# Optimization experiments

Hardware: AMD Instinct MI355X
Metric: run time of the kernel (lower is better)

Reference implementation:

```python
import jax, jax.numpy as jnp
import numpy as np

B = 8192
EPS = 1e-5  # BatchNorm eps (torch default)


def binarize(x):
    # sign binarization with straight-through estimator (matches the .data trick
    # in BinarizeConv2d/BinarizeLinear: forward sees +-1, backward sees identity)
    s = jnp.where(x >= 0, 1.0, -1.0).astype(x.dtype)
    return x + jax.lax.stop_gradient(s - x)


def conv2d(x, w, stride, pad):
    return jax.lax.conv_general_dilated(
        x, w, window_strides=stride, padding=pad,
        dimension_numbers=('NCHW', 'OIHW', 'NCHW'))


def bn(x, g, b, m, v):
    # eval-mode BatchNorm2d folded into one scale+shift per channel
    inv = g * jax.lax.rsqrt(v + EPS)
    return x * inv[None, :, None, None] + (b - m * inv)[None, :, None, None]


def maxpool_w2(x):
    # MaxPool2d(kernel=(1,2), stride=(1,2))
    return jax.lax.reduce_window(x, -jnp.inf, jax.lax.max,
                                 (1, 1, 1, 2), (1, 1, 1, 2), 'VALID')


def setup_inputs() -> dict:
    key = jax.random.key(0)
    ks = jax.random.split(key, 32)
    d = {}
    d['x'] = jax.random.normal(ks[0], (B, 1, 6, 128), jnp.float32)

    def w(k, shape):
        return jax.random.normal(k, shape, jnp.float32) * 0.05

    # conv weights (OIHW) and biases
    d['w1'] = w(ks[1], (32, 1, 1, 9));    d['b1'] = w(ks[2], (32,))
    d['w2'] = w(ks[3], (64, 32, 1, 3));   d['b2'] = w(ks[4], (64,))
    d['w3'] = w(ks[5], (128, 64, 1, 3));  d['b3'] = w(ks[6], (128,))
    d['w4'] = w(ks[7], (128, 128, 6, 1)); d['b4'] = w(ks[8], (128,))
    # BatchNorm params (gamma, beta, running_mean, running_var)
    for i, c in zip((1, 2, 3, 4), (32, 64, 128, 128)):
        kk = jax.random.split(ks[8 + i], 4)
        d[f'g{i}'] = 1.0 + 0.1 * jax.random.normal(kk[0], (c,), jnp.float32)
        d[f'be{i}'] = 0.1 * jax.random.normal(kk[1], (c,), jnp.float32)
        d[f'm{i}'] = 0.1 * jax.random.normal(kk[2], (c,), jnp.float32)
        d[f'v{i}'] = jax.random.uniform(kk[3], (c,), jnp.float32, 0.5, 1.5)
    # fc: BinarizeLinear(2048, 10)
    d['wf'] = w(ks[20], (10, 2048))
    d['bf'] = w(ks[21], (10,))
    return d


def reference(x, w1, b1, w2, b2, w3, b3, w4, b4,
              g1, be1, m1, v1, g2, be2, m2, v2,
              g3, be3, m3, v3, g4, be4, m4, v4, wf, bf):
    # block 1: first layer keeps real-valued input, binarized weights
    h = conv2d(x, binarize(w1), (1, 2), [(0, 0), (4, 4)]) + b1[None, :, None, None]
    h = jnp.clip(bn(h, g1, be1, m1, v1), -1.0, 1.0)   # Hardtanh
    h = maxpool_w2(h)                                  # [B,32,6,32]
    # block 2: binarized activations + weights
    h = conv2d(binarize(h), binarize(w2), (1, 1), [(0, 0), (1, 1)]) + b2[None, :, None, None]
    h = jnp.clip(bn(h, g2, be2, m2, v2), -1.0, 1.0)    # [B,64,6,32]
    # block 3
    h = conv2d(binarize(h), binarize(w3), (1, 1), [(0, 0), (1, 1)]) + b3[None, :, None, None]
    h = jnp.clip(bn(h, g3, be3, m3, v3), -1.0, 1.0)
    h = maxpool_w2(h)                                  # [B,128,6,16]
    # block 4: (6,1) kernel collapses H
    h = conv2d(binarize(h), binarize(w4), (1, 1), [(0, 0), (0, 0)]) + b4[None, :, None, None]
    h = jnp.clip(bn(h, g4, be4, m4, v4), -1.0, 1.0)    # [B,128,1,16]
    h = h.reshape(h.shape[0], -1)                      # [B,2048]
    return binarize(h) @ binarize(wf).T + bf           # [B,10]
```

## Files before the change

kernel.cpp:

```cpp
#include <hip/hip_runtime.h>
#include <cstdint>
#include <cstddef>

#define BN_EPS 1e-5f
#define BATCH 8192

typedef unsigned long long u64;
typedef uint32_t u32;
typedef int v4i __attribute__((ext_vector_type(4)));
typedef int v16i __attribute__((ext_vector_type(16)));

__device__ __forceinline__ u32 f2k(float f) {
    u32 u = __float_as_uint(f);
    return (u >> 31) ? ~u : (u | 0x80000000u);
}
__device__ __forceinline__ float k2f(u32 k) {
    u32 u = (k & 0x80000000u) ? (k ^ 0x80000000u) : ~k;
    return __uint_as_float(u);
}
__device__ __forceinline__ float bn_eval(float conv, float B, float iv, float sh) {
    return __fadd_rn(__fmul_rn(__fadd_rn(conv, B), iv), sh);
}

__global__ __launch_bounds__(256) void prep_all(
    const float* w1, const float* b1, const float* w2, const float* b2,
    const float* w3, const float* b3, const float* w4, const float* b4,
    const float* wf,
    const float* g1, const float* be1, const float* m1, const float* v1,
    const float* g2, const float* be2, const float* m2, const float* v2,
    const float* g3, const float* be3, const float* m3, const float* v3,
    const float* g4, const float* be4, const float* m4, const float* v4,
    float* s1f, float* T1, u32* wt2w, int* T2,
    uint4* b3i8, int* C3, u64* wt4, int* T4, u64* wtf) {
    int t = blockIdx.x * 256 + threadIdx.x;

    if (t < 384) {
        int co = t / 12, k = t % 12;
        float val = 0.f;
        if (k < 9) {
            float iv = g1[co] * rsqrtf(v1[co] + BN_EPS);
            float d = (iv < 0.f) ? -1.f : 1.f;
            val = ((w1[co * 9 + k] >= 0.f) ? 1.f : -1.f) * d;
        }
        s1f[t] = val;
    } else if (t < 416) {
        int co = t - 384;
        float iv = g1[co] * rsqrtf(v1[co] + BN_EPS);
        float sh = be1[co] - m1[co] * iv;
        float B = b1[co];
        bool flip = (iv < 0.f);
        auto pred = [&](float sp) {
            float sum = flip ? -sp : sp;
            return bn_eval(sum, B, iv, sh) >= 0.f;
        };
        u32 lo = f2k(-3.0e38f), hi = f2k(3.0e38f);
        float Tv;
        if (pred(k2f(lo))) Tv = k2f(lo);
        else if (!pred(k2f(hi))) Tv = __uint_as_float(0x7F800000u);
        else {
            while (hi - lo > 1u) {
                u32 mid = lo + ((hi - lo) >> 1);
                if (pred(k2f(mid))) hi = mid; else lo = mid;
            }
            Tv = k2f(hi);
        }
        T1[co] = Tv;
    } else if (t < 608) {
        int idx = t - 416;
        int co = idx / 3, kw = idx % 3;
        float iv = g2[co] * rsqrtf(v2[co] + BN_EPS);
        bool flip = (iv < 0.f);
        u32 wb = 0;
        for (int ci = 0; ci < 32; ++ci)
            wb |= (u32)((w2[(co * 32 + ci) * 3 + kw] >= 0.f) != flip) << ci;
        wt2w[co * 4 + kw] = wb;
    } else if (t < 800) {
        int idx = t - 608;
        int co = idx & 63, cls = idx >> 6;
        float iv = g2[co] * rsqrtf(v2[co] + BN_EPS);
        float sh = be2[co] - m2[co] * iv;
        float B = b2[co];
        bool flip = (iv < 0.f);
        int spur = 0, nv = 3;
        if (cls == 1) { nv = 2; for (int ci = 0; ci < 32; ++ci) spur += (int)((w2[(co * 32 + ci) * 3 + 0] >= 0.f) != flip); }
        if (cls == 2) { nv = 2; for (int ci = 0; ci < 32; ++ci) spur += (int)((w2[(co * 32 + ci) * 3 + 2] >= 0.f) != flip); }
        int maxp = 32 * nv + spur;
        int T = -1;
        for (int p = 0; p <= maxp; ++p) {
            int conv = flip ? (2 * (p - spur) - 32 * nv) : (32 * nv - 2 * (p - spur));
            float y = bn_eval((float)conv, B, iv, sh);
            if ((y >= 0.f) && (T == p - 1)) T = p;
        }
        T2[cls * 64 + co] = T;
    } else if (t < 2336) {
        int idx = t - 800;
        int q = idx >> 7, n = idx & 127;
        float iv = g3[n] * rsqrtf(v3[n] + BN_EPS);
        bool flip = (iv < 0.f);
        int kw = q >> 2, ci0 = (q & 3) * 16;
        u32 wd[4] = {0, 0, 0, 0};
        for (int j = 0; j < 16; ++j) {
            int ci = ci0 + j;
            bool pos = (w3[(n * 64 + ci) * 3 + kw] >= 0.f) != flip;
            u32 byte = pos ? 0x01u : 0xFFu;
            wd[j >> 2] |= byte << (8 * (j & 3));
        }
        b3i8[idx] = make_uint4(wd[0], wd[1], wd[2], wd[3]);
    } else if (t < 2464) {
        int co = t - 2336;
        float iv = g3[co] * rsqrtf(v3[co] + BN_EPS);
        float sh = be3[co] - m3[co] * iv;
        float B = b3[co];
        int C = 1000;
        if (iv >= 0.f) {
            for (int v = -192; v <= 192; v += 2)
                if (bn_eval((float)v, B, iv, sh) >= 0.f) { C = v; break; }
        } else {
            for (int v = 192; v >= -192; v -= 2)
                if (bn_eval((float)v, B, iv, sh) >= 0.f) { C = -v; break; }
        }
        C3[co] = C;
    } else if (t < 4000) {
        int idx = t - 2464;
        int j = idx & 1, ch = idx >> 1;
        int co = ch / 6, h = ch % 6;
        float iv = g4[co] * rsqrtf(v4[co] + BN_EPS);
        bool flip = (iv < 0.f);
        u64 wb = 0;
        for (int cb = 0; cb < 64; ++cb) {
            int ci = j * 64 + cb;
            wb |= (u64)((w4[(co * 128 + ci) * 6 + h] >= 0.f) != flip) << cb;
        }
        wt4[idx] = wb;
    } else if (t < 4128) {
        int co = t - 4000;
        float iv = g4[co] * rsqrtf(v4[co] + BN_EPS);
        float sh = be4[co] - m4[co] * iv;
        float B = b4[co];
        bool flip = (iv < 0.f);
        int T = -1;
        for (int p = 0; p <= 768; ++p) {
            int conv = flip ? (2 * p - 768) : (768 - 2 * p);
            float y = bn_eval((float)conv, B, iv, sh);
            if ((y >= 0.f) && (T == p - 1)) T = p;
        }
        T4[co] = T;
    } else if (t < 4448) {
        int idx = t - 4128;
        int o = idx / 32, wi = idx % 32;
        u64 wb = 0;
        for (int fb = 0; fb < 64; ++fb)
            wb |= (u64)(wf[o * 2048 + wi * 64 + fb] >= 0.f) << fb;
        wtf[idx] = wb;
    }
}

#define L12_ROWS 8
__global__ __launch_bounds__(256) void layer12_kernel(
    const float* __restrict__ x, const float4* __restrict__ s1p, const float* __restrict__ T1,
    const uint4* __restrict__ wt2v, const int* __restrict__ T2, u64* __restrict__ a2) {
    __shared__ float4 sS[96];
    __shared__ float sT[32];
    __shared__ uint4 sW[64];
    __shared__ int sT2[192];
    __shared__ u32 sA1[L12_ROWS][32];
    int t = threadIdx.x;
    if (t < 96) sS[t] = s1p[t];
    if (t < 32) sT[t] = T1[t];
    if (t < 64) sW[t] = wt2v[t];
    if (t < 192) sT2[t] = T2[t];
    __syncthreads();

    int r = t >> 5, wp = t & 31;
    int bh = blockIdx.x * L12_ROWS + r;
    const float* xp = x + (size_t)bh * 128;
    float xv[11];
    int p0 = 4 * wp - 4;
#pragma unroll
    for (int j = 0; j < 11; ++j) {
        int p = p0 + j;
        xv[j] = (p >= 0 && p < 128) ? xp[p] : 0.f;
    }
    u32 word = 0;
#pragma unroll
    for (int co = 0; co < 32; ++co) {
        float4 wa = sS[co * 3 + 0];
        float4 wb = sS[co * 3 + 1];
        float wc = sS[co * 3 + 2].x;
        float sum0 = 0.f, sum1 = 0.f;
        sum0 = fmaf(wa.x, xv[0], sum0);  sum1 = fmaf(wa.x, xv[2], sum1);
        sum0 = fmaf(wa.y, xv[1], sum0);  sum1 = fmaf(wa.y, xv[3], sum1);
        sum0 = fmaf(wa.z, xv[2], sum0);  sum1 = fmaf(wa.z, xv[4], sum1);
        sum0 = fmaf(wa.w, xv[3], sum0);  sum1 = fmaf(wa.w, xv[5], sum1);
        sum0 = fmaf(wb.x, xv[4], sum0);  sum1 = fmaf(wb.x, xv[6], sum1);
        sum0 = fmaf(wb.y, xv[5], sum0);  sum1 = fmaf(wb.y, xv[7], sum1);
        sum0 = fmaf(wb.z, xv[6], sum0);  sum1 = fmaf(wb.z, xv[8], sum1);
        sum0 = fmaf(wb.w, xv[7], sum0);  sum1 = fmaf(wb.w, xv[9], sum1);
        sum0 = fmaf(wc,   xv[8], sum0);  sum1 = fmaf(wc,   xv[10], sum1);
        float Tt = sT[co];
        word |= (u32)((sum0 >= Tt) || (sum1 >= Tt)) << co;
    }
    sA1[r][wp] = word;
    __syncthreads();

    u32 am = sA1[r][wp];
    u32 al = (wp > 0) ? sA1[r][wp - 1] : 0u;
    u32 ar = (wp < 31) ? sA1[r][wp + 1] : 0u;
    const int* Tp = &sT2[(wp == 0) ? 64 : ((wp == 31) ? 128 : 0)];
    u64 word2 = 0;
#pragma unroll
    for (int co = 0; co < 64; ++co) {
        uint4 wv = sW[co];
        int p = __popc(al ^ wv.x) + __popc(am ^ wv.y) + __popc(ar ^ wv.z);
        word2 |= (u64)(p <= Tp[co]) << co;
    }
    a2[(size_t)bh * 32 + wp] = word2;
}

#define L3_ROWS 4
__global__ __launch_bounds__(256) void layer3_mfma(
    const u64* __restrict__ a2, const uint4* __restrict__ b3i8, const int* __restrict__ C3,
    u32* __restrict__ a3u32) {
    __shared__ uint4 sB[12 * 128];
    __shared__ u64 sLUT[256];
    __shared__ int sC3[128];
    int t = threadIdx.x;
    for (int i = t; i < 1536; i += 256) sB[i] = b3i8[i];
    {
        u32 b = t & 255;
        u64 e = 0;
#pragma unroll
        for (int j = 0; j < 8; ++j)
            e |= (((b >> j) & 1) ? 0x01ull : 0xFFull) << (8 * j);
        if (t < 256) sLUT[t] = e;
    }
    if (t < 128) sC3[t] = C3[t];
    __syncthreads();

    int wv = t >> 6, lane = t & 63, m = lane & 31, half = lane >> 5;
    int rowBase = (blockIdx.x * 4 + wv) * L3_ROWS;
    const int prTab[8] = {0, 1, 4, 5, 8, 9, 12, 13};

    for (int r = 0; r < L3_ROWS; ++r) {
        int bh = rowBase + r;
        u64 aw = a2[(size_t)bh * 32 + m];
        u64 wm1 = __shfl(aw, m - 1);
        u64 wp1 = __shfl(aw, m + 1);

        v4i A[6];
#pragma unroll
        for (int kk = 0; kk < 6; ++kk) {
            const int kw = kk >> 1;
            u64 word = (kw == 0) ? wm1 : ((kw == 1) ? aw : wp1);
            bool valid = !((kw == 0 && m == 0) || (kw == 2 && m == 31));
            int ci0 = ((kk & 1) << 5) + (half << 4);
            u32 bits = (u32)(word >> ci0) & 0xFFFFu;
            u64 lo = sLUT[bits & 0xFF];
            u64 hi = sLUT[bits >> 8];
            if (!valid) { lo = 0; hi = 0; }
            union { u64 q[2]; v4i v; } u;
            u.q[0] = lo; u.q[1] = hi;
            A[kk] = u.v;
        }

        u32 outv = 0;
#pragma unroll
        for (int nt = 0; nt < 4; ++nt) {
            v16i acc;
#pragma unroll
            for (int i = 0; i < 16; ++i) acc[i] = 0;
#pragma unroll
            for (int kk = 0; kk < 6; ++kk) {
                int q = kk * 2 + half;
                union { uint4 u4; v4i v; } bu;
                bu.u4 = sB[q * 128 + nt * 32 + m];
                acc = __builtin_amdgcn_mfma_i32_32x32x32_i8(A[kk], bu.v, acc, 0, 0, 0);
            }
            int tc = sC3[nt * 32 + m];
#pragma unroll
            for (int rp = 0; rp < 8; ++rp) {
                bool c = (acc[2 * rp] >= tc) || (acc[2 * rp + 1] >= tc);
                u64 mk = __ballot(c);
                int LA = (nt << 4) | prTab[rp];
                int LB = LA + 2;
                outv = (lane == LA) ? (u32)mk : outv;
                outv = (lane == LB) ? (u32)(mk >> 32) : outv;
            }
        }
        a3u32[(size_t)bh * 64 + ((lane & 15) << 2) + (lane >> 4)] = outv;
    }
}

__global__ __launch_bounds__(256) void layer4_fc_kernel(
    const u64* __restrict__ a3, const u64* __restrict__ wt4, const int* __restrict__ T4,
    const u64* __restrict__ wtf, const float* __restrict__ bf, float* __restrict__ out) {
    __shared__ u64 sW4[1536];
    __shared__ u64 sWf[320];
    __shared__ u64 sFeat[16][32];
    __shared__ int sT[128];
    __shared__ float sBf[10];
    int t = threadIdx.x;
    {
        ulonglong2* d = (ulonglong2*)sW4;
        const ulonglong2* s = (const ulonglong2*)wt4;
        for (int i = t; i < 768; i += 256) d[i] = s[i];
        ulonglong2* df = (ulonglong2*)sWf;
        const ulonglong2* sf = (const ulonglong2*)wtf;
        if (t < 160) df[t] = sf[t];
    }
    if (t < 128) sT[t] = T4[t];
    if (t < 10) sBf[t] = bf[t];
    __syncthreads();
    int bb = t >> 4, w = t & 15, lane = t & 63, g = lane >> 4;
    int b = blockIdx.x * 16 + bb;
    u64 av[12];
#pragma unroll
    for (int h = 0; h < 6; ++h) {
        av[h * 2 + 0] = a3[(size_t)b * 192 + h * 32 + w * 2 + 0];
        av[h * 2 + 1] = a3[(size_t)b * 192 + h * 32 + w * 2 + 1];
    }
    u64 acc = 0;
#pragma unroll 8
    for (int co = 0; co < 128; ++co) {
        const u64* wr = &sW4[co * 12];
        int p = 0;
#pragma unroll
        for (int q = 0; q < 12; ++q) p += __popcll(av[q] ^ wr[q]);
        u64 m = __ballot(p <= sT[co]);
        u64 field = (m >> (g * 16)) & 0xFFFFull;
        acc |= field << ((co & 3) << 4);
        if ((co & 3) == 3) {
            if (w == 0) sFeat[bb][co >> 2] = acc;
            acc = 0;
        }
    }
    __syncthreads();
    if (t < 160) {
        int fb = t / 10, o = t % 10;
        int p = 0;
#pragma unroll
        for (int wi = 0; wi < 32; ++wi) p += __popcll(sFeat[fb][wi] ^ sWf[o * 32 + wi]);
        out[(size_t)(blockIdx.x * 16 + fb) * 10 + o] = __fadd_rn((float)(2048 - 2 * p), sBf[o]);
    }
}

extern "C" void kernel_launch(void* const* d_in, const int* in_sizes, int n_in,
                              void* d_out, int out_size, void* d_ws, size_t ws_size,
                              hipStream_t stream) {
    const float* x  = (const float*)d_in[0];
    const float* w1 = (const float*)d_in[1];  const float* b1 = (const float*)d_in[2];
    const float* w2 = (const float*)d_in[3];  const float* b2 = (const float*)d_in[4];
    const float* w3 = (const float*)d_in[5];  const float* b3 = (const float*)d_in[6];
    const float* w4 = (const float*)d_in[7];  const float* b4 = (const float*)d_in[8];
    const float* g1 = (const float*)d_in[9];  const float* be1 = (const float*)d_in[10];
    const float* m1 = (const float*)d_in[11]; const float* v1 = (const float*)d_in[12];
    const float* g2 = (const float*)d_in[13]; const float* be2 = (const float*)d_in[14];
    const float* m2 = (const float*)d_in[15]; const float* v2 = (const float*)d_in[16];
    const float* g3 = (const float*)d_in[17]; const float* be3 = (const float*)d_in[18];
    const float* m3 = (const float*)d_in[19]; const float* v3 = (const float*)d_in[20];
    const float* g4 = (const float*)d_in[21]; const float* be4 = (const float*)d_in[22];
    const float* m4 = (const float*)d_in[23]; const float* v4 = (const float*)d_in[24];
    const float* wf = (const float*)d_in[25]; const float* bf = (const float*)d_in[26];
    float* out = (float*)d_out;

    char* ws = (char*)d_ws;
    u64* a2 = (u64*)(ws + 0);
    u64* a3 = (u64*)(ws + 12582912);
    const size_t S = 25165824;
    uint4* b3i8 = (uint4*)(ws + S + 0);
    u64*  wt4  = (u64*) (ws + S + 24576);
    u64*  wtf  = (u64*) (ws + S + 36864);
    u32*  wt2w = (u32*) (ws + S + 39424);
    float* s1f = (float*)(ws + S + 40448);
    float* T1  = (float*)(ws + S + 41984);
    int*  T2   = (int*)  (ws + S + 42112);
    int*  C3   = (int*)  (ws + S + 42880);
    int*  T4   = (int*)  (ws + S + 43392);

    prep_all<<<18, 256, 0, stream>>>(w1, b1, w2, b2, w3, b3, w4, b4, wf,
                                     g1, be1, m1, v1, g2, be2, m2, v2,
                                     g3, be3, m3, v3, g4, be4, m4, v4,
                                     s1f, T1, wt2w, T2, b3i8, C3, wt4, T4, wtf);

    layer12_kernel<<<(BATCH * 6) / L12_ROWS, 256, 0, stream>>>(
        x, (const float4*)s1f, T1, (const uint4*)wt2w, T2, a2);
    layer3_mfma<<<(BATCH * 6) / (4 * L3_ROWS), 256, 0, stream>>>(a2, b3i8, C3, (u32*)a3);
    layer4_fc_kernel<<<BATCH / 16, 256, 0, stream>>>(a3, wt4, T4, wtf, bf, out);
}
```

Baseline: 283.8 us.

## Fuse layer3 MFMA with layer4/fc and restructure layer1 per-channel threads

Merges the layer3 MFMA kernel and the layer4+fc kernel into one kernel, so each block computes 96 rows of layer3 activations into shared memory and consumes them directly. This removes the a3 round trip through global memory and one launch. Layer1 is also reorganised so each thread owns one output channel with weights in registers, sliding a window over an input row staged in shared memory, and ballot packs the bit words. The fused kernel uses much more shared memory and launches only 512 blocks, which may reduce occupancy and latency hiding.

```diff
diff --git a/kernel.cpp b/kernel.cpp
--- a/kernel.cpp
+++ b/kernel.cpp
@@ -159,71 +159,82 @@
 __global__ __launch_bounds__(256) void layer12_kernel(
     const float* __restrict__ x, const float4* __restrict__ s1p, const float* __restrict__ T1,
     const uint4* __restrict__ wt2v, const int* __restrict__ T2, u64* __restrict__ a2) {
-    __shared__ float4 sS[96];
-    __shared__ float sT[32];
+    __shared__ float sX[L12_ROWS][144];
+    __shared__ u32 sA1[L12_ROWS][32];
     __shared__ uint4 sW[64];
     __shared__ int sT2[192];
-    __shared__ u32 sA1[L12_ROWS][32];
     int t = threadIdx.x;
-    if (t < 96) sS[t] = s1p[t];
-    if (t < 32) sT[t] = T1[t];
+    int bh0 = blockIdx.x * L12_ROWS;
+    for (int i = t; i < L12_ROWS * 144; i += 256) {
+        int r = i / 144, c = i % 144;
+        float v = 0.f;
+        if (c >= 4 && c < 132) v = x[(size_t)(bh0 + r) * 128 + (c - 4)];
+        sX[r][c] = v;
+    }
     if (t < 64) sW[t] = wt2v[t];
     if (t < 192) sT2[t] = T2[t];
+
+    int co = t & 31, rr = t >> 5, lane = t & 63;
+    float4 wa = s1p[co * 3 + 0];
+    float4 wb = s1p[co * 3 + 1];
+    float wc = s1p[co * 3 + 2].x;
+    float Tt = T1[co];
+    __syncthreads();
+
+    const float* xr = sX[rr];
+    float4 A0 = *(const float4*)&xr[0];
+    float4 A1 = *(const float4*)&xr[4];
+    float4 A2 = *(const float4*)&xr[8];
+    u32 myword = 0;
+    for (int wp = 0; wp < 32; ++wp) {
+        float sum0 = 0.f, sum1 = 0.f;
+        sum0 = fmaf(wa.x, A0.x, sum0);  sum1 = fmaf(wa.x, A0.z, sum1);
+        sum0 = fmaf(wa.y, A0.y, sum0);  sum1 = fmaf(wa.y, A0.w, sum1);
+        sum0 = fmaf(wa.z, A0.z, sum0);  sum1 = fmaf(wa.z, A1.x, sum1);
+        sum0 = fmaf(wa.w, A0.w, sum0);  sum1 = fmaf(wa.w, A1.y, sum1);
+        sum0 = fmaf(wb.x, A1.x, sum0);  sum1 = fmaf(wb.x, A1.z, sum1);
+        sum0 = fmaf(wb.y, A1.y, sum0);  sum1 = fmaf(wb.y, A1.w, sum1);
+        sum0 = fmaf(wb.z, A1.z, sum0);  sum1 = fmaf(wb.z, A2.x, sum1);
+        sum0 = fmaf(wb.w, A1.w, sum0);  sum1 = fmaf(wb.w, A2.y, sum1);
+        sum0 = fmaf(wc,   A2.x, sum0);  sum1 = fmaf(wc,   A2.z, sum1);
+        bool pred = (sum0 >= Tt) || (sum1 >= Tt);
+        u64 mk = __ballot(pred);
+        u32 hw = (lane < 32) ? (u32)mk : (u32)(mk >> 32);
+        if ((lane & 31) == wp) myword = hw;
+        A0 = A1; A1 = A2;
+        A2 = *(const float4*)&xr[4 * wp + 12];
+    }
+    sA1[((t >> 6) << 1) + (lane >> 5)][lane & 31] = myword;
     __syncthreads();
 
     int r = t >> 5, wp = t & 31;
-    int bh = blockIdx.x * L12_ROWS + r;
-    const float* xp = x + (size_t)bh * 128;
-    float xv[11];
-    int p0 = 4 * wp - 4;
-#pragma unroll
-    for (int j = 0; j < 11; ++j) {
-        int p = p0 + j;
-        xv[j] = (p >= 0 && p < 128) ? xp[p] : 0.f;
-    }
-    u32 word = 0;
-#pragma unroll
-    for (int co = 0; co < 32; ++co) {
-        float4 wa = sS[co * 3 + 0];
-        float4 wb = sS[co * 3 + 1];
-        float wc = sS[co * 3 + 2].x;
-        float sum0 = 0.f, sum1 = 0.f;
-        sum0 = fmaf(wa.x, xv[0], sum0);  sum1 = fmaf(wa.x, xv[2], sum1);
-        sum0 = fmaf(wa.y, xv[1], sum0);  sum1 = fmaf(wa.y, xv[3], sum1);
-        sum0 = fmaf(wa.z, xv[2], sum0);  sum1 = fmaf(wa.z, xv[4], sum1);
-        sum0 = fmaf(wa.w, xv[3], sum0);  sum1 = fmaf(wa.w, xv[5], sum1);
-        sum0 = fmaf(wb.x, xv[4], sum0);  sum1 = fmaf(wb.x, xv[6], sum1);
-        sum0 = fmaf(wb.y, xv[5], sum0);  sum1 = fmaf(wb.y, xv[7], sum1);
-        sum0 = fmaf(wb.z, xv[6], sum0);  sum1 = fmaf(wb.z, xv[8], sum1);
-        sum0 = fmaf(wb.w, xv[7], sum0);  sum1 = fmaf(wb.w, xv[9], sum1);
-        sum0 = fmaf(wc,   xv[8], sum0);  sum1 = fmaf(wc,   xv[10], sum1);
-        float Tt = sT[co];
-        word |= (u32)((sum0 >= Tt) || (sum1 >= Tt)) << co;
-    }
-    sA1[r][wp] = word;
-    __syncthreads();
-
     u32 am = sA1[r][wp];
     u32 al = (wp > 0) ? sA1[r][wp - 1] : 0u;
     u32 ar = (wp < 31) ? sA1[r][wp + 1] : 0u;
     const int* Tp = &sT2[(wp == 0) ? 64 : ((wp == 31) ? 128 : 0)];
     u64 word2 = 0;
 #pragma unroll
-    for (int co = 0; co < 64; ++co) {
-        uint4 wv = sW[co];
+    for (int c = 0; c < 64; ++c) {
+        uint4 wv = sW[c];
         int p = __popc(al ^ wv.x) + __popc(am ^ wv.y) + __popc(ar ^ wv.z);
-        word2 |= (u64)(p <= Tp[co]) << co;
-    }
-    a2[(size_t)bh * 32 + wp] = word2;
-}
-
-#define L3_ROWS 4
-__global__ __launch_bounds__(256) void layer3_mfma(
+        word2 |= (u64)(p <= Tp[c]) << c;
+    }
+    a2[(size_t)(bh0 + r) * 32 + wp] = word2;
+}
+
+__global__ __launch_bounds__(256) void layer34_kernel(
     const u64* __restrict__ a2, const uint4* __restrict__ b3i8, const int* __restrict__ C3,
-    u32* __restrict__ a3u32) {
+    const u64* __restrict__ wt4, const int* __restrict__ T4,
+    const u64* __restrict__ wtf, const float* __restrict__ bf, float* __restrict__ out) {
     __shared__ uint4 sB[12 * 128];
     __shared__ u64 sLUT[256];
     __shared__ int sC3[128];
+    __shared__ u64 sA3[96 * 33];
+    __shared__ u64 sW4[1536];
+    __shared__ u64 sWf[320];
+    __shared__ u64 sFeat[16][32];
+    __shared__ int sT[128];
+    __shared__ float sBf[10];
     int t = threadIdx.x;
     for (int i = t; i < 1536; i += 256) sB[i] = b3i8[i];
     {
@@ -235,14 +246,24 @@
         if (t < 256) sLUT[t] = e;
     }
     if (t < 128) sC3[t] = C3[t];
+    {
+        ulonglong2* d = (ulonglong2*)sW4;
+        const ulonglong2* s = (const ulonglong2*)wt4;
+        for (int i = t; i < 768; i += 256) d[i] = s[i];
+        ulonglong2* df = (ulonglong2*)sWf;
+        const ulonglong2* sf = (const ulonglong2*)wtf;
+        if (t < 160) df[t] = sf[t];
+    }
+    if (t < 128) sT[t] = T4[t];
+    if (t < 10) sBf[t] = bf[t];
     __syncthreads();
 
     int wv = t >> 6, lane = t & 63, m = lane & 31, half = lane >> 5;
-    int rowBase = (blockIdx.x * 4 + wv) * L3_ROWS;
     const int prTab[8] = {0, 1, 4, 5, 8, 9, 12, 13};
-
-    for (int r = 0; r < L3_ROWS; ++r) {
-        int bh = rowBase + r;
+    u32* sA3u = (u32*)sA3;
+    for (int r = 0; r < 24; ++r) {
+        int rl = wv * 24 + r;
+        int bh = blockIdx.x * 96 + rl;
         u64 aw = a2[(size_t)bh * 32 + m];
         u64 wm1 = __shfl(aw, m - 1);
         u64 wp1 = __shfl(aw, m + 1);
@@ -287,50 +308,29 @@
                 outv = (lane == LB) ? (u32)(mk >> 32) : outv;
             }
         }
-        a3u32[(size_t)bh * 64 + ((lane & 15) << 2) + (lane >> 4)] = outv;
-    }
-}
-
-__global__ __launch_bounds__(256) void layer4_fc_kernel(
-    const u64* __restrict__ a3, const u64* __restrict__ wt4, const int* __restrict__ T4,
-    const u64* __restrict__ wtf, const float* __restrict__ bf, float* __restrict__ out) {
-    __shared__ u64 sW4[1536];
-    __shared__ u64 sWf[320];
-    __shared__ u64 sFeat[16][32];
-    __shared__ int sT[128];
-    __shared__ float sBf[10];
-    int t = threadIdx.x;
-    {
-        ulonglong2* d = (ulonglong2*)sW4;
-        const ulonglong2* s = (const ulonglong2*)wt4;
-        for (int i = t; i < 768; i += 256) d[i] = s[i];
-        ulonglong2* df = (ulonglong2*)sWf;
-        const ulonglong2* sf = (const ulonglong2*)wtf;
-        if (t < 160) df[t] = sf[t];
-    }
-    if (t < 128) sT[t] = T4[t];
-    if (t < 10) sBf[t] = bf[t];
-    __syncthreads();
-    int bb = t >> 4, w = t & 15, lane = t & 63, g = lane >> 4;
-    int b = blockIdx.x * 16 + bb;
+        sA3u[rl * 66 + ((lane & 15) << 2) + (lane >> 4)] = outv;
+    }
+    __syncthreads();
+
+    int bb = t >> 4, w = t & 15, g = lane >> 4;
     u64 av[12];
 #pragma unroll
     for (int h = 0; h < 6; ++h) {
-        av[h * 2 + 0] = a3[(size_t)b * 192 + h * 32 + w * 2 + 0];
-        av[h * 2 + 1] = a3[(size_t)b * 192 + h * 32 + w * 2 + 1];
+        av[h * 2 + 0] = sA3[(bb * 6 + h) * 33 + w * 2 + 0];
+        av[h * 2 + 1] = sA3[(bb * 6 + h) * 33 + w * 2 + 1];
     }
     u64 acc = 0;
 #pragma unroll 8
-    for (int co = 0; co < 128; ++co) {
-        const u64* wr = &sW4[co * 12];
+    for (int c = 0; c < 128; ++c) {
+        const u64* wr = &sW4[c * 12];
         int p = 0;
 #pragma unroll
         for (int q = 0; q < 12; ++q) p += __popcll(av[q] ^ wr[q]);
-        u64 m = __ballot(p <= sT[co]);
-        u64 field = (m >> (g * 16)) & 0xFFFFull;
-        acc |= field << ((co & 3) << 4);
-        if ((co & 3) == 3) {
-            if (w == 0) sFeat[bb][co >> 2] = acc;
+        u64 mk = __ballot(p <= sT[c]);
+        u64 field = (mk >> (g * 16)) & 0xFFFFull;
+        acc |= field << ((c & 3) << 4);
+        if ((c & 3) == 3) {
+            if (w == 0) sFeat[bb][c >> 2] = acc;
             acc = 0;
         }
     }
@@ -365,8 +365,7 @@
 
     char* ws = (char*)d_ws;
     u64* a2 = (u64*)(ws + 0);
-    u64* a3 = (u64*)(ws + 12582912);
-    const size_t S = 25165824;
+    const size_t S = 12582912;
     uint4* b3i8 = (uint4*)(ws + S + 0);
     u64*  wt4  = (u64*) (ws + S + 24576);
     u64*  wtf  = (u64*) (ws + S + 36864);
@@ -384,6 +383,5 @@
 
     layer12_kernel<<<(BATCH * 6) / L12_ROWS, 256, 0, stream>>>(
         x, (const float4*)s1f, T1, (const uint4*)wt2w, T2, a2);
-    layer3_mfma<<<(BATCH * 6) / (4 * L3_ROWS), 256, 0, stream>>>(a2, b3i8, C3, (u32*)a3);
-    layer4_fc_kernel<<<BATCH / 16, 256, 0, stream>>>(a3, wt4, T4, wtf, bf, out);
-}
+    layer34_kernel<<<BATCH / 16, 256, 0, stream>>>(a2, b3i8, C3, wt4, T4, wtf, bf, out);
+}
```

After: 280.9 us. No clear change (-1.0%).
